# Kernel tuning notes

Hardware: AMD Instinct MI355X
Metric: run time of the kernel (lower is better)

## Reference

```python
import jax, jax.numpy as jnp
import numpy as np
import math

B, S, H = 2, 2048, 2048
NQ, NKV, HD = 16, 4, 128
THETA = 10000.0


def rotate_half(x):
    x1, x2 = jnp.split(x, 2, axis=-1)
    return jnp.concatenate([-x2, x1], axis=-1)


def rope_cos_sin(position_ids, dim, base, dtype):
    # inv_freq: (dim/2,)
    inv_freq = 1.0 / (base ** (jnp.arange(0, dim, 2, dtype=jnp.float32) / dim))
    freqs = position_ids.astype(jnp.float32)[..., None] * inv_freq  # (B, S, dim/2)
    emb = jnp.concatenate([freqs, freqs], axis=-1)  # (B, S, dim)
    return jnp.cos(emb).astype(dtype), jnp.sin(emb).astype(dtype)


def setup_inputs() -> dict:
    key = jax.random.key(0)
    ks = jax.random.split(key, 5)
    hidden_states = jax.random.normal(ks[0], (B, S, H), dtype=jnp.float32)
    position_ids = jnp.broadcast_to(jnp.arange(S, dtype=jnp.int32)[None, :], (B, S))
    sc = 0.02
    wq = jax.random.normal(ks[1], (NQ * HD, H), dtype=jnp.float32) * sc
    wk = jax.random.normal(ks[2], (NKV * HD, H), dtype=jnp.float32) * sc
    wv = jax.random.normal(ks[3], (NKV * HD, H), dtype=jnp.float32) * sc
    wo = jax.random.normal(ks[4], (H, NQ * HD), dtype=jnp.float32) * sc
    return {"hidden_states": hidden_states, "position_ids": position_ids,
            "wq": wq, "wk": wk, "wv": wv, "wo": wo}


def reference(hidden_states, position_ids, wq, wk, wv, wo):
    b, s, _ = hidden_states.shape
    n_rep = NQ // NKV
    # QKV projections (no bias)
    q = (hidden_states @ wq.T).reshape(b, s, NQ, HD).transpose(0, 2, 1, 3)   # (b, nq, s, hd)
    k = (hidden_states @ wk.T).reshape(b, s, NKV, HD).transpose(0, 2, 1, 3)  # (b, nkv, s, hd)
    v = (hidden_states @ wv.T).reshape(b, s, NKV, HD).transpose(0, 2, 1, 3)
    # RoPE (full rotary, partial_rotary_factor == 1.0)
    cos, sin = rope_cos_sin(position_ids, HD, THETA, q.dtype)  # (b, s, hd)
    cos = cos[:, None, :, :]
    sin = sin[:, None, :, :]
    q = q * cos + rotate_half(q) * sin
    k = k * cos + rotate_half(k) * sin
    # repeat_kv for GQA: (b, nkv, s, hd) -> (b, nq, s, hd)
    k = jnp.repeat(k, n_rep, axis=1)
    v = jnp.repeat(v, n_rep, axis=1)
    # scores (b, nq, s, s)
    scores = jnp.einsum('bhqd,bhkd->bhqk', q, k) / math.sqrt(HD)
    causal = jnp.triu(jnp.full((s, s), -jnp.inf, dtype=scores.dtype), k=1)
    scores = scores + causal
    probs = jax.nn.softmax(scores.astype(jnp.float32), axis=-1).astype(q.dtype)
    out = jnp.einsum('bhqk,bhkd->bhqd', probs, v)  # (b, nq, s, hd)
    out = out.transpose(0, 2, 1, 3).reshape(b, s, NQ * HD)
    return out @ wo.T
```

## Files before the change

### kernel.cpp

```cpp
#include <hip/hip_runtime.h>
#include <hip/hip_bf16.h>
#include <cstdint>

typedef unsigned short u16;
typedef __attribute__((ext_vector_type(4))) float f32x4;
typedef __attribute__((ext_vector_type(8))) short s16x8;
typedef __attribute__((ext_vector_type(4))) unsigned int u32x4;
typedef __attribute__((ext_vector_type(2))) unsigned int u32x2;
typedef __attribute__((ext_vector_type(4))) unsigned short u16x4;
typedef __attribute__((ext_vector_type(8))) unsigned short u16x8;

#define MFMA16(a, b, c) __builtin_amdgcn_mfma_f32_16x16x32_bf16(a, b, c, 0, 0, 0)
#define GLOAD16(g, l) __builtin_amdgcn_global_load_lds((const __attribute__((address_space(1))) void*)(g), (__attribute__((address_space(3))) void*)(l), 16, 0, 0)

__device__ __forceinline__ u16 f2bf(float f) {
    union { float f; uint32_t u; } v{f};
    uint32_t r = v.u + 0x7FFF + ((v.u >> 16) & 1);
    return (u16)(r >> 16);
}
__device__ __forceinline__ float bf2f(u16 b) {
    union { uint32_t u; float f; } v;
    v.u = ((uint32_t)b) << 16;
    return v.f;
}

__global__ void cast_all(const float* __restrict__ h, const float* __restrict__ wq,
                         const float* __restrict__ wk, const float* __restrict__ wv,
                         const float* __restrict__ wo, u16* __restrict__ Xb,
                         u16* __restrict__ WB, u16* __restrict__ WoB) {
    int i = blockIdx.x * 256 + threadIdx.x;
    const float* src; u16* dst; int off;
    if (i < 2097152)      { src = h;  dst = Xb;           off = i; }
    else if (i < 3145728) { src = wq; dst = WB;           off = i - 2097152; }
    else if (i < 3407872) { src = wk; dst = WB + 4194304; off = i - 3145728; }
    else if (i < 3670016) { src = wv; dst = WB + 5242880; off = i - 3407872; }
    else                  { src = wo; dst = WoB;          off = i - 3670016; }
    float4 f = ((const float4*)src)[off];
    u16x4 o = { f2bf(f.x), f2bf(f.y), f2bf(f.z), f2bf(f.w) };
    ((u16x4*)dst)[off] = o;
}

__global__ void rope_table_k(const int* __restrict__ pos, float* __restrict__ ct, float* __restrict__ st) {
    int i = blockIdx.x * 256 + threadIdx.x;
    int j = i & 63;
    int bs = i >> 6;
    float p = (float)pos[bs];
    float invf = powf(10000.0f, -(float)j * (1.0f / 64.0f));
    float ang = p * invf;
    ct[i] = cosf(ang);
    st[i] = sinf(ang);
}

template <int FUSE>
__global__ __launch_bounds__(256) void gemm_bt(const u16* __restrict__ A, const u16* __restrict__ Bw,
                                               float* __restrict__ C, int M, int N, int K,
                                               const float* __restrict__ ct, const float* __restrict__ st,
                                               u16* __restrict__ Qb, u16* __restrict__ Kb,
                                               u16* __restrict__ Vb) {
    __shared__ u16 Sh[32768];
    const int tid = threadIdx.x;
    const int lane = tid & 63, wid = tid >> 6;
    const int g = lane >> 4, r = lane & 15;

    const int gx = gridDim.x, nwg = gx * gridDim.y;
    int lid = blockIdx.y * gx + blockIdx.x;
    int swz = (lid % 8) * (nwg / 8) + lid / 8;
    const int bxi = swz % gx, byi = swz / gx;

    const size_t bm = (size_t)byi * 128, bn = (size_t)bxi * 128;
    const int wr = (wid >> 1) * 64, wc = (wid & 1) * 64;

    const int srow = wid * 32 + (lane >> 3);
    const int schunk = (lane & 7) ^ ((lane >> 3) & 7);
    const u16* aSrc = A + (bm + srow) * (size_t)K + schunk * 8;
    const u16* bSrc = Bw + (bn + srow) * (size_t)K + schunk * 8;

    auto STAGE = [&](int ktEl, int bi) {
        u16* aD = Sh + bi * 16384 + wid * 2048;
        u16* bD = Sh + bi * 16384 + 8192 + wid * 2048;
#pragma unroll
        for (int j = 0; j < 4; ++j) {
            GLOAD16(aSrc + (size_t)(j * 8) * K + ktEl, aD + j * 512);
            GLOAD16(bSrc + (size_t)(j * 8) * K + ktEl, bD + j * 512);
        }
    };

    f32x4 acc[4][4] = {};
    const int nk = K >> 6;
    STAGE(0, 0);
    __syncthreads();
    for (int t = 0; t < nk; ++t) {
        if (t + 1 < nk) STAGE((t + 1) << 6, (t + 1) & 1);
        const u16* As = Sh + (t & 1) * 16384;
        const u16* Bs = As + 8192;
        s16x8 af[4][2], bfr[4][2];
#pragma unroll
        for (int m = 0; m < 4; ++m)
#pragma unroll
            for (int kk = 0; kk < 2; ++kk) {
                int rowa = wr + m * 16 + r;
                af[m][kk] = *(const s16x8*)(As + rowa * 64 + (((kk * 4 + g) ^ (rowa & 7)) << 3));
                int rowb = wc + m * 16 + r;
                bfr[m][kk] = *(const s16x8*)(Bs + rowb * 64 + (((kk * 4 + g) ^ (rowb & 7)) << 3));
            }
#pragma unroll
        for (int m = 0; m < 4; ++m)
#pragma unroll
            for (int n = 0; n < 4; ++n) {
                acc[m][n] = MFMA16(af[m][0], bfr[n][0], acc[m][n]);
                acc[m][n] = MFMA16(af[m][1], bfr[n][1], acc[m][n]);
            }
        __syncthreads();
    }
    if (FUSE == 0) {
#pragma unroll
        for (int m = 0; m < 4; ++m)
#pragma unroll
            for (int n = 0; n < 4; ++n)
#pragma unroll
                for (int i = 0; i < 4; ++i) {
                    size_t row = bm + wr + m * 16 + g * 4 + i;
                    size_t col = bn + wc + n * 16 + r;
                    C[row * N + col] = acc[m][n][i];
                }
        return;
    }
    const int hb = bxi;
    if (hb < 20) {
#pragma unroll
        for (int m = 0; m < 4; ++m)
#pragma unroll
            for (int n = 0; n < 4; ++n)
#pragma unroll
                for (int i = 0; i < 4; ++i) {
                    int rowl = wr + m * 16 + g * 4 + i;
                    int col = wc + n * 16 + r;
                    int c4 = col >> 3;
                    *(u16*)((char*)Sh + rowl * 256 + (((c4 ^ (rowl & 15))) << 4) + ((col & 7) << 1)) =
                        f2bf(acc[m][n][i]);
                }
        __syncthreads();
        if (tid < 128) {
            const int rowl = tid;
            const size_t tok = bm + rowl;
            const int b = (int)(tok >> 11), s = (int)(tok & 2047);
            u16* dst;
            if (hb < 16) dst = Qb + (((size_t)(b * 16 + hb) * 2048 + s) << 7);
            else         dst = Kb + (((size_t)(b * 4 + (hb - 16)) * 2048 + s) << 7);
            const char* tb = (const char*)Sh + rowl * 256;
            const float* ctr = ct + tok * 64;
            const float* str = st + tok * 64;
#pragma unroll
            for (int c4 = 0; c4 < 8; ++c4) {
                u32x4 lo4 = *(const u32x4*)(tb + ((c4 ^ (rowl & 15)) << 4));
                u32x4 hi4 = *(const u32x4*)(tb + (((c4 + 8) ^ (rowl & 15)) << 4));
                const u16* lo = (const u16*)&lo4;
                const u16* hi = (const u16*)&hi4;
                u16x4 o0, o1, o2, o3;
                u16* olo[2] = { (u16*)&o0, (u16*)&o1 };
                u16* ohi[2] = { (u16*)&o2, (u16*)&o3 };
#pragma unroll
                for (int j = 0; j < 8; ++j) {
                    float c = ctr[c4 * 8 + j], sn = str[c4 * 8 + j];
                    float xl = bf2f(lo[j]), xh = bf2f(hi[j]);
                    olo[j >> 2][j & 3] = f2bf(xl * c - xh * sn);
                    ohi[j >> 2][j & 3] = f2bf(xh * c + xl * sn);
                }
                *(u16x4*)(dst + c4 * 8) = o0;
                *(u16x4*)(dst + c4 * 8 + 4) = o1;
                *(u16x4*)(dst + 64 + c4 * 8) = o2;
                *(u16x4*)(dst + 64 + c4 * 8 + 4) = o3;
            }
        }
    } else {
#pragma unroll
        for (int m = 0; m < 4; ++m) {
            int tokb = wr + m * 16 + g * 4;
            int chunk = tokb >> 3;
            int sub = (g & 1) * 8;
#pragma unroll
            for (int n = 0; n < 4; ++n) {
                int d = wc + n * 16 + r;
                u16x4 v = { f2bf(acc[m][n][0]), f2bf(acc[m][n][1]),
                            f2bf(acc[m][n][2]), f2bf(acc[m][n][3]) };
                *(u16x4*)((char*)Sh + d * 256 + (((chunk ^ (d & 15))) << 4) + sub) = v;
            }
        }
        __syncthreads();
        const int b = (int)(bm >> 11), s0 = (int)(bm & 2047);
        u16* dst = Vb + (size_t)(b * 4 + (hb - 20)) * 262144;
        const int dd = tid >> 1, half = (tid & 1) * 8;
#pragma unroll
        for (int c8 = 0; c8 < 8; ++c8) {
            int sc = half + c8;
            u32x4 v4 = *(const u32x4*)((const char*)Sh + dd * 256 + (((sc ^ (dd & 15))) << 4));
            *(u32x4*)(dst + (size_t)dd * 2048 + s0 + sc * 8) = v4;
        }
    }
}

__global__ __launch_bounds__(256, 2) void attn_k(const u16* __restrict__ Qb, const u16* __restrict__ Kb,
                                                 const u16* __restrict__ Vb, u16* __restrict__ Ob) {
    __shared__ char smem[49152];
    u16* Ksh = (u16*)smem;
    u16* Vts = (u16*)(smem + 16384);
    char* Pall = smem + 32768;
    const int tid = threadIdx.x;
    const int lane = tid & 63, w = tid >> 6;
    const int g = lane >> 4, r = lane & 15;

    const int lid = blockIdx.y * gridDim.x + blockIdx.x;
    const int cpy = lid >> 8, p = lid & 255;
    const int bh = p & 31;
    const int qblk = cpy ? (7 - (p >> 5)) : ((p >> 5) + 8);

    const int b = bh >> 4, h = bh & 15;
    const int hkv = h >> 2;
    const int q0 = qblk * 128;
    const u16* Qh = Qb + ((size_t)(b * 16 + h) << 18);
    const u16* Kh = Kb + ((size_t)(b * 4 + hkv) << 18);
    const u16* Vh = Vb + ((size_t)(b * 4 + hkv) << 18);

    s16x8 qf[2][4];
#pragma unroll
    for (int qq = 0; qq < 2; ++qq)
#pragma unroll
        for (int c = 0; c < 4; ++c)
            qf[qq][c] = *(const s16x8*)(Qh + (size_t)(q0 + qq * 64 + w * 16 + r) * 128 + c * 32 + g * 8);

    f32x4 o[2][8] = {};
    float mrun[2] = {-1e30f, -1e30f};
    float lrun[2] = {0.f, 0.f};
    const int fmax[2] = { q0 + w * 16 + 15, q0 + 64 + w * 16 + 15 };

    const int ntiles = 2 * qblk + 2;
    const int krow0 = tid >> 4, kch = tid & 15;

    u32x4 kpr[4], vpr[4];
#pragma unroll
    for (int it = 0; it < 4; ++it)
        kpr[it] = *(const u32x4*)(Kh + (size_t)(krow0 + it * 16) * 128 + kch * 8);
#pragma unroll
    for (int it = 0; it < 4; ++it) {
        int task = tid + it * 256;
        vpr[it] = *(const u32x4*)(Vh + (size_t)(task >> 3) * 2048 + (task & 7) * 8);
    }

    for (int t = 0; t < ntiles; ++t) {
        const int kv0 = t * 64;
        __syncthreads();
#pragma unroll
        for (int it = 0; it < 4; ++it) {
            int row = krow0 + it * 16;
            *(u32x4*)((char*)Ksh + row * 256 + ((kch ^ (row & 7)) << 4)) = kpr[it];
        }
#pragma unroll
        for (int it = 0; it < 4; ++it) {
            int task = tid + it * 256;
            int d = task >> 3, ch = task & 7;
            *(u32x4*)((char*)Vts + d * 128 + ((ch ^ (d & 7) ^ ((d >> 3) & 7)) << 4)) = vpr[it];
        }
        if (t + 1 < ntiles) {
            const int kn = kv0 + 64;
#pragma unroll
            for (int it = 0; it < 4; ++it)
                kpr[it] = *(const u32x4*)(Kh + (size_t)(kn + krow0 + it * 16) * 128 + kch * 8);
#pragma unroll
            for (int it = 0; it < 4; ++it) {
                int task = tid + it * 256;
                vpr[it] = *(const u32x4*)(Vh + (size_t)(task >> 3) * 2048 + kn + (task & 7) * 8);
            }
        }
        __syncthreads();
        f32x4 st4[2][4];
#pragma unroll
        for (int ts = 0; ts < 4; ++ts) {
            int row = ts * 16 + r;
            s16x8 kf[4];
#pragma unroll
            for (int c = 0; c < 4; ++c)
                kf[c] = *(const s16x8*)((const char*)Ksh + row * 256 + (((c * 4 + g) ^ (row & 7)) << 4));
            f32x4 a0 = {}, a1 = {};
            if (kv0 <= fmax[0])
#pragma unroll
                for (int c = 0; c < 4; ++c) a0 = MFMA16(kf[c], qf[0][c], a0);
            if (kv0 <= fmax[1])
#pragma unroll
                for (int c = 0; c < 4; ++c) a1 = MFMA16(kf[c], qf[1][c], a1);
            st4[0][ts] = a0;
            st4[1][ts] = a1;
        }
#pragma unroll
        for (int qq = 0; qq < 2; ++qq) {
            if (kv0 > fmax[qq]) continue;
            const int qg = q0 + qq * 64 + w * 16 + r;
            float sv[16];
            float mtile = -1e30f;
#pragma unroll
            for (int ts = 0; ts < 4; ++ts)
#pragma unroll
                for (int i = 0; i < 4; ++i) {
                    int kvg = kv0 + ts * 16 + g * 4 + i;
                    float s = st4[qq][ts][i] * 0.08838834764831845f;
                    s = (kvg > qg) ? -1e30f : s;
                    sv[ts * 4 + i] = s;
                    mtile = fmaxf(mtile, s);
                }
            mtile = fmaxf(mtile, __shfl_xor(mtile, 16));
            mtile = fmaxf(mtile, __shfl_xor(mtile, 32));
            float mold = mrun[qq];
            if (!__all(mtile <= mold + 8.0f)) {
                float mnew = fmaxf(mold, mtile);
                float corr = __expf(mold - mnew);
#pragma unroll
                for (int dsb = 0; dsb < 8; ++dsb)
#pragma unroll
                    for (int i = 0; i < 4; ++i) o[qq][dsb][i] *= corr;
                lrun[qq] *= corr;
                mrun[qq] = mnew;
            }
            float mm = mrun[qq];
            float psum = 0.f;
            unsigned int pw[8];
#pragma unroll
            for (int ts = 0; ts < 4; ++ts) {
                float p0 = __expf(sv[ts * 4 + 0] - mm);
                float p1 = __expf(sv[ts * 4 + 1] - mm);
                float p2 = __expf(sv[ts * 4 + 2] - mm);
                float p3 = __expf(sv[ts * 4 + 3] - mm);
                psum += (p0 + p1) + (p2 + p3);
                pw[ts * 2 + 0] = (unsigned int)f2bf(p0) | ((unsigned int)f2bf(p1) << 16);
                pw[ts * 2 + 1] = (unsigned int)f2bf(p2) | ((unsigned int)f2bf(p3) << 16);
            }
            psum += __shfl_xor(psum, 16);
            psum += __shfl_xor(psum, 32);
            lrun[qq] += psum;
            char* pbase = Pall + (w * 2 + qq) * 2048;
#pragma unroll
            for (int ts = 0; ts < 4; ++ts) {
                int chunk = (ts * 2 + (g >> 1)) ^ (r & 7);
                u32x2 val = { pw[ts * 2], pw[ts * 2 + 1] };
                *(u32x2*)(pbase + r * 128 + chunk * 16 + (g & 1) * 8) = val;
            }
        }
        asm volatile("s_waitcnt lgkmcnt(0)" ::: "memory");
#pragma unroll
        for (int c = 0; c < 2; ++c) {
            s16x8 vf[8];
#pragma unroll
            for (int dsb = 0; dsb < 8; ++dsb) {
                int d = dsb * 16 + r;
                vf[dsb] = *(const s16x8*)((const char*)Vts + d * 128 +
                    ((((c * 4 + g) ^ (d & 7) ^ ((d >> 3) & 7))) << 4));
            }
#pragma unroll
            for (int qq = 0; qq < 2; ++qq) {
                if (kv0 > fmax[qq]) continue;
                s16x8 pf = *(const s16x8*)(Pall + (w * 2 + qq) * 2048 + r * 128 +
                                           (((c * 4 + g) ^ (r & 7)) << 4));
#pragma unroll
                for (int dsb = 0; dsb < 8; ++dsb)
                    o[qq][dsb] = MFMA16(vf[dsb], pf, o[qq][dsb]);
            }
        }
    }
    __syncthreads();
#pragma unroll
    for (int qq = 0; qq < 2; ++qq) {
        float linv = 1.0f / lrun[qq];
        char* obase = smem + (w << 13) + (qq << 12);
#pragma unroll
        for (int dsb = 0; dsb < 8; ++dsb)
#pragma unroll
            for (int i = 0; i < 4; ++i) {
                int d = dsb * 16 + g * 4 + i;
                *(u16*)(obase + r * 256 + d * 2) = f2bf(o[qq][dsb][i] * linv);
            }
    }
    asm volatile("s_waitcnt lgkmcnt(0)" ::: "memory");
    const int rr = lane >> 2, cbo = (lane & 3) * 32;
#pragma unroll
    for (int qq = 0; qq < 2; ++qq) {
        char* obase = smem + (w << 13) + (qq << 12);
        size_t oidx = ((size_t)b * 2048 + q0 + qq * 64 + w * 16 + rr) * 2048 + h * 128 + cbo;
#pragma unroll
        for (int p2 = 0; p2 < 4; ++p2) {
            u32x4 vv = *(const u32x4*)(obase + rr * 256 + cbo * 2 + p2 * 16);
            *(u32x4*)(Ob + oidx + p2 * 8) = vv;
        }
    }
}

extern "C" void kernel_launch(void* const* d_in, const int* in_sizes, int n_in,
                              void* d_out, int out_size, void* d_ws, size_t ws_size,
                              hipStream_t stream) {
    const float* hidden = (const float*)d_in[0];
    const int* pos = (const int*)d_in[1];
    const float* wq = (const float*)d_in[2];
    const float* wk = (const float*)d_in[3];
    const float* wv = (const float*)d_in[4];
    const float* wo = (const float*)d_in[5];
    float* out = (float*)d_out;

    char* ws = (char*)d_ws;
    size_t off = 0;
    auto alloc = [&](size_t bytes) { char* p = ws + off; off += (bytes + 255) & ~255ULL; return p; };
    u16* Xb   = (u16*)alloc(8388608ULL * 2);
    u16* WB   = (u16*)alloc(6291456ULL * 2);
    u16* WoB  = (u16*)alloc(4194304ULL * 2);
    u16* Qb   = (u16*)alloc(8388608ULL * 2);
    u16* Kb   = (u16*)alloc(2097152ULL * 2);
    u16* Vb   = (u16*)alloc(2097152ULL * 2);
    u16* Ab   = (u16*)alloc(8388608ULL * 2);
    float* ctab = (float*)alloc(262144ULL * 4);
    float* stab = (float*)alloc(262144ULL * 4);

    cast_all<<<18432, 256, 0, stream>>>(hidden, wq, wk, wv, wo, Xb, WB, WoB);
    rope_table_k<<<1024, 256, 0, stream>>>(pos, ctab, stab);
    gemm_bt<1><<<dim3(24, 32), 256, 0, stream>>>(Xb, WB, nullptr, 4096, 3072, 2048,
                                                 ctab, stab, Qb, Kb, Vb);
    attn_k<<<dim3(16, 32), 256, 0, stream>>>(Qb, Kb, Vb, Ab);
    gemm_bt<0><<<dim3(16, 32), 256, 0, stream>>>(Ab, WoB, out, 4096, 2048, 2048,
                                                 nullptr, nullptr, nullptr, nullptr, nullptr);
}
```

Baseline: 234.2 us.

## Widen attention KV tile to 128 and read V fragments directly from global

The attention kernel now processes 128 keys per iteration instead of 64, halving the number of loop iterations and block-wide barriers. K staging in LDS grows to fill 128 rows, and the P scratch buffers double in size, bringing shared memory to 64 KB. V is no longer prefetched and staged in LDS; each wave loads its V MFMA operands straight from global memory. The per-tile causal MFMA skip for QK is also dropped. The trade-off is fewer syncs and less LDS traffic against global-load latency on V that is no longer hidden by prefetching, strided V accesses, more LDS per block, and higher register pressure.

```diff
diff --git a/kernel.cpp b/kernel.cpp
--- a/kernel.cpp
+++ b/kernel.cpp
@@ -201,9 +201,8 @@
 
 __global__ __launch_bounds__(256, 2) void attn_k(const u16* __restrict__ Qb, const u16* __restrict__ Kb,
                                                  const u16* __restrict__ Vb, u16* __restrict__ Ob) {
-    __shared__ char smem[49152];
+    __shared__ char smem[65536];
     u16* Ksh = (u16*)smem;
-    u16* Vts = (u16*)(smem + 16384);
     char* Pall = smem + 32768;
     const int tid = threadIdx.x;
     const int lane = tid & 63, w = tid >> 6;
@@ -233,60 +232,43 @@
     float lrun[2] = {0.f, 0.f};
     const int fmax[2] = { q0 + w * 16 + 15, q0 + 64 + w * 16 + 15 };
 
-    const int ntiles = 2 * qblk + 2;
+    const int ntiles = qblk + 1;
     const int krow0 = tid >> 4, kch = tid & 15;
 
-    u32x4 kpr[4], vpr[4];
-#pragma unroll
-    for (int it = 0; it < 4; ++it)
+    u32x4 kpr[8];
+#pragma unroll
+    for (int it = 0; it < 8; ++it)
         kpr[it] = *(const u32x4*)(Kh + (size_t)(krow0 + it * 16) * 128 + kch * 8);
-#pragma unroll
-    for (int it = 0; it < 4; ++it) {
-        int task = tid + it * 256;
-        vpr[it] = *(const u32x4*)(Vh + (size_t)(task >> 3) * 2048 + (task & 7) * 8);
-    }
 
     for (int t = 0; t < ntiles; ++t) {
-        const int kv0 = t * 64;
+        const int kv0 = t * 128;
         __syncthreads();
 #pragma unroll
-        for (int it = 0; it < 4; ++it) {
+        for (int it = 0; it < 8; ++it) {
             int row = krow0 + it * 16;
             *(u32x4*)((char*)Ksh + row * 256 + ((kch ^ (row & 7)) << 4)) = kpr[it];
         }
-#pragma unroll
-        for (int it = 0; it < 4; ++it) {
-            int task = tid + it * 256;
-            int d = task >> 3, ch = task & 7;
-            *(u32x4*)((char*)Vts + d * 128 + ((ch ^ (d & 7) ^ ((d >> 3) & 7)) << 4)) = vpr[it];
-        }
         if (t + 1 < ntiles) {
-            const int kn = kv0 + 64;
-#pragma unroll
-            for (int it = 0; it < 4; ++it)
+            const int kn = kv0 + 128;
+#pragma unroll
+            for (int it = 0; it < 8; ++it)
                 kpr[it] = *(const u32x4*)(Kh + (size_t)(kn + krow0 + it * 16) * 128 + kch * 8);
-#pragma unroll
-            for (int it = 0; it < 4; ++it) {
-                int task = tid + it * 256;
-                vpr[it] = *(const u32x4*)(Vh + (size_t)(task >> 3) * 2048 + kn + (task & 7) * 8);
-            }
         }
         __syncthreads();
-        f32x4 st4[2][4];
-#pragma unroll
-        for (int ts = 0; ts < 4; ++ts) {
+        f32x4 st4[2][8];
+#pragma unroll
+        for (int ts = 0; ts < 8; ++ts) {
             int row = ts * 16 + r;
             s16x8 kf[4];
 #pragma unroll
             for (int c = 0; c < 4; ++c)
                 kf[c] = *(const s16x8*)((const char*)Ksh + row * 256 + (((c * 4 + g) ^ (row & 7)) << 4));
             f32x4 a0 = {}, a1 = {};
-            if (kv0 <= fmax[0])
-#pragma unroll
-                for (int c = 0; c < 4; ++c) a0 = MFMA16(kf[c], qf[0][c], a0);
-            if (kv0 <= fmax[1])
-#pragma unroll
-                for (int c = 0; c < 4; ++c) a1 = MFMA16(kf[c], qf[1][c], a1);
+#pragma unroll
+            for (int c = 0; c < 4; ++c) {
+                a0 = MFMA16(kf[c], qf[0][c], a0);
+                a1 = MFMA16(kf[c], qf[1][c], a1);
+            }
             st4[0][ts] = a0;
             st4[1][ts] = a1;
         }
@@ -294,10 +276,10 @@
         for (int qq = 0; qq < 2; ++qq) {
             if (kv0 > fmax[qq]) continue;
             const int qg = q0 + qq * 64 + w * 16 + r;
-            float sv[16];
+            float sv[32];
             float mtile = -1e30f;
 #pragma unroll
-            for (int ts = 0; ts < 4; ++ts)
+            for (int ts = 0; ts < 8; ++ts)
 #pragma unroll
                 for (int i = 0; i < 4; ++i) {
                     int kvg = kv0 + ts * 16 + g * 4 + i;
@@ -321,42 +303,38 @@
             }
             float mm = mrun[qq];
             float psum = 0.f;
-            unsigned int pw[8];
-#pragma unroll
-            for (int ts = 0; ts < 4; ++ts) {
-                float p0 = __expf(sv[ts * 4 + 0] - mm);
-                float p1 = __expf(sv[ts * 4 + 1] - mm);
-                float p2 = __expf(sv[ts * 4 + 2] - mm);
-                float p3 = __expf(sv[ts * 4 + 3] - mm);
-                psum += (p0 + p1) + (p2 + p3);
-                pw[ts * 2 + 0] = (unsigned int)f2bf(p0) | ((unsigned int)f2bf(p1) << 16);
-                pw[ts * 2 + 1] = (unsigned int)f2bf(p2) | ((unsigned int)f2bf(p3) << 16);
+            unsigned int pw[16];
+#pragma unroll
+            for (int t2 = 0; t2 < 16; ++t2) {
+                float p0 = __expf(sv[t2 * 2] - mm);
+                float p1 = __expf(sv[t2 * 2 + 1] - mm);
+                psum += p0 + p1;
+                pw[t2] = (unsigned)f2bf(p0) | ((unsigned)f2bf(p1) << 16);
             }
             psum += __shfl_xor(psum, 16);
             psum += __shfl_xor(psum, 32);
             lrun[qq] += psum;
-            char* pbase = Pall + (w * 2 + qq) * 2048;
-#pragma unroll
-            for (int ts = 0; ts < 4; ++ts) {
+            char* pbase = Pall + (w * 2 + qq) * 4096;
+#pragma unroll
+            for (int ts = 0; ts < 8; ++ts) {
                 int chunk = (ts * 2 + (g >> 1)) ^ (r & 7);
                 u32x2 val = { pw[ts * 2], pw[ts * 2 + 1] };
-                *(u32x2*)(pbase + r * 128 + chunk * 16 + (g & 1) * 8) = val;
+                *(u32x2*)(pbase + r * 256 + chunk * 16 + (g & 1) * 8) = val;
             }
         }
         asm volatile("s_waitcnt lgkmcnt(0)" ::: "memory");
 #pragma unroll
-        for (int c = 0; c < 2; ++c) {
+        for (int c = 0; c < 4; ++c) {
             s16x8 vf[8];
 #pragma unroll
             for (int dsb = 0; dsb < 8; ++dsb) {
                 int d = dsb * 16 + r;
-                vf[dsb] = *(const s16x8*)((const char*)Vts + d * 128 +
-                    ((((c * 4 + g) ^ (d & 7) ^ ((d >> 3) & 7))) << 4));
+                vf[dsb] = *(const s16x8*)(Vh + (size_t)d * 2048 + kv0 + c * 32 + g * 8);
             }
 #pragma unroll
             for (int qq = 0; qq < 2; ++qq) {
                 if (kv0 > fmax[qq]) continue;
-                s16x8 pf = *(const s16x8*)(Pall + (w * 2 + qq) * 2048 + r * 128 +
+                s16x8 pf = *(const s16x8*)(Pall + (w * 2 + qq) * 4096 + r * 256 +
                                            (((c * 4 + g) ^ (r & 7)) << 4));
 #pragma unroll
                 for (int dsb = 0; dsb < 8; ++dsb)
```

Result: slower. 291.9 us (+24.6%).

## Double-buffer K tiles in LDS and restructure attention loop synchronization

Applied to the files above, without the earlier changes.

The attention kernel now keeps two K tile buffers in shared memory. The next K tile is written to the alternate buffer right after the QK^T MFMAs, and the V tile is refilled after the PV stage, so register prefetch runs two tiles ahead. This moves loads and LDS writes between compute phases to overlap memory latency with MFMA work. It also raises shared memory from 48KB to 64KB per block, which may limit the two-blocks-per-CU occupancy, and the loop still has two barriers per iteration.

```diff
diff --git a/kernel.cpp b/kernel.cpp
--- a/kernel.cpp
+++ b/kernel.cpp
@@ -201,10 +201,9 @@
 
 __global__ __launch_bounds__(256, 2) void attn_k(const u16* __restrict__ Qb, const u16* __restrict__ Kb,
                                                  const u16* __restrict__ Vb, u16* __restrict__ Ob) {
-    __shared__ char smem[49152];
-    u16* Ksh = (u16*)smem;
-    u16* Vts = (u16*)(smem + 16384);
-    char* Pall = smem + 32768;
+    __shared__ char smem[65536];
+    u16* Vts = (u16*)(smem + 32768);
+    char* Pall = smem + 49152;
     const int tid = threadIdx.x;
     const int lane = tid & 63, w = tid >> 6;
     const int g = lane >> 4, r = lane & 15;
@@ -245,33 +244,32 @@
         int task = tid + it * 256;
         vpr[it] = *(const u32x4*)(Vh + (size_t)(task >> 3) * 2048 + (task & 7) * 8);
     }
+#pragma unroll
+    for (int it = 0; it < 4; ++it) {
+        int row = krow0 + it * 16;
+        *(u32x4*)(smem + row * 256 + ((kch ^ (row & 7)) << 4)) = kpr[it];
+    }
+#pragma unroll
+    for (int it = 0; it < 4; ++it) {
+        int task = tid + it * 256;
+        int d = task >> 3, ch = task & 7;
+        *(u32x4*)((char*)Vts + d * 128 + ((ch ^ (d & 7) ^ ((d >> 3) & 7)) << 4)) = vpr[it];
+    }
+    if (ntiles > 1) {
+#pragma unroll
+        for (int it = 0; it < 4; ++it)
+            kpr[it] = *(const u32x4*)(Kh + (size_t)(64 + krow0 + it * 16) * 128 + kch * 8);
+#pragma unroll
+        for (int it = 0; it < 4; ++it) {
+            int task = tid + it * 256;
+            vpr[it] = *(const u32x4*)(Vh + (size_t)(task >> 3) * 2048 + 64 + (task & 7) * 8);
+        }
+    }
+    __syncthreads();
 
     for (int t = 0; t < ntiles; ++t) {
         const int kv0 = t * 64;
-        __syncthreads();
-#pragma unroll
-        for (int it = 0; it < 4; ++it) {
-            int row = krow0 + it * 16;
-            *(u32x4*)((char*)Ksh + row * 256 + ((kch ^ (row & 7)) << 4)) = kpr[it];
-        }
-#pragma unroll
-        for (int it = 0; it < 4; ++it) {
-            int task = tid + it * 256;
-            int d = task >> 3, ch = task & 7;
-            *(u32x4*)((char*)Vts + d * 128 + ((ch ^ (d & 7) ^ ((d >> 3) & 7)) << 4)) = vpr[it];
-        }
-        if (t + 1 < ntiles) {
-            const int kn = kv0 + 64;
-#pragma unroll
-            for (int it = 0; it < 4; ++it)
-                kpr[it] = *(const u32x4*)(Kh + (size_t)(kn + krow0 + it * 16) * 128 + kch * 8);
-#pragma unroll
-            for (int it = 0; it < 4; ++it) {
-                int task = tid + it * 256;
-                vpr[it] = *(const u32x4*)(Vh + (size_t)(task >> 3) * 2048 + kn + (task & 7) * 8);
-            }
-        }
-        __syncthreads();
+        const char* kb = smem + ((t & 1) << 14);
         f32x4 st4[2][4];
 #pragma unroll
         for (int ts = 0; ts < 4; ++ts) {
@@ -279,7 +277,7 @@
             s16x8 kf[4];
 #pragma unroll
             for (int c = 0; c < 4; ++c)
-                kf[c] = *(const s16x8*)((const char*)Ksh + row * 256 + (((c * 4 + g) ^ (row & 7)) << 4));
+                kf[c] = *(const s16x8*)(kb + row * 256 + (((c * 4 + g) ^ (row & 7)) << 4));
             f32x4 a0 = {}, a1 = {};
             if (kv0 <= fmax[0])
 #pragma unroll
@@ -289,6 +287,20 @@
                 for (int c = 0; c < 4; ++c) a1 = MFMA16(kf[c], qf[1][c], a1);
             st4[0][ts] = a0;
             st4[1][ts] = a1;
+        }
+        if (t + 1 < ntiles) {
+            char* kbn = smem + (((t + 1) & 1) << 14);
+#pragma unroll
+            for (int it = 0; it < 4; ++it) {
+                int row = krow0 + it * 16;
+                *(u32x4*)(kbn + row * 256 + ((kch ^ (row & 7)) << 4)) = kpr[it];
+            }
+            if (t + 2 < ntiles) {
+                const int kn2 = kv0 + 128;
+#pragma unroll
+                for (int it = 0; it < 4; ++it)
+                    kpr[it] = *(const u32x4*)(Kh + (size_t)(kn2 + krow0 + it * 16) * 128 + kch * 8);
+            }
         }
 #pragma unroll
         for (int qq = 0; qq < 2; ++qq) {
@@ -363,8 +375,25 @@
                     o[qq][dsb] = MFMA16(vf[dsb], pf, o[qq][dsb]);
             }
         }
-    }
-    __syncthreads();
+        __syncthreads();
+        if (t + 1 < ntiles) {
+#pragma unroll
+            for (int it = 0; it < 4; ++it) {
+                int task = tid + it * 256;
+                int d = task >> 3, ch = task & 7;
+                *(u32x4*)((char*)Vts + d * 128 + ((ch ^ (d & 7) ^ ((d >> 3) & 7)) << 4)) = vpr[it];
+            }
+            if (t + 2 < ntiles) {
+                const int kn2 = kv0 + 128;
+#pragma unroll
+                for (int it = 0; it < 4; ++it) {
+                    int task = tid + it * 256;
+                    vpr[it] = *(const u32x4*)(Vh + (size_t)(task >> 3) * 2048 + kn2 + (task & 7) * 8);
+                }
+            }
+        }
+        __syncthreads();
+    }
 #pragma unroll
     for (int qq = 0; qq < 2; ++qq) {
         float linv = 1.0f / lrun[qq];
```

Result: no change. 231.6 us (-1.1%).
